# Optimization experiments

Hardware: AMD Instinct MI355X
Metric: run time of the kernel (lower is better)

## Reference

```python
import jax, jax.numpy as jnp
import numpy as np

B, N, H, NH = 1024, 101, 128, 8
HD = H // NH
EPS = 1e-5  # torch LayerNorm default


def _xavier(k, shape):
    fan_in, fan_out = shape
    lim = float(np.sqrt(6.0 / (fan_in + fan_out)))
    return jax.random.uniform(k, shape, jnp.float32, -lim, lim)


def setup_inputs() -> dict:
    key = jax.random.key(0)
    ks = jax.random.split(key, 12)
    return {
        "encoder_inputs": jax.random.normal(ks[0], (B, N, H), jnp.float32),
        "pool": jax.random.normal(ks[1], (B, H), jnp.float32),
        "capacity": jnp.ones((B, 1), jnp.float32),
        "demand": jax.random.uniform(ks[2], (B, N), jnp.float32),
        "fc_w": _xavier(ks[3], (H + 1, H)),      # nn.Linear(hidden+1, hidden, bias=False), stored [in,out]
        "fc1_w": _xavier(ks[4], (H, H)),
        "dec_ln_g": jnp.ones((H,), jnp.float32),
        "dec_ln_b": jnp.zeros((H,), jnp.float32),
        "wq": _xavier(ks[5], (H, H)),             # TransformerAttention q/k/v/out projections
        "wk": _xavier(ks[6], (H, H)),
        "wv": _xavier(ks[7], (H, H)),
        "wo": _xavier(ks[8], (H, H)),
        "kp_w": _xavier(ks[9], (H, H)),           # pointer self.k
        "ptr_ln_g": jnp.ones((H,), jnp.float32),
        "ptr_ln_b": jnp.zeros((H,), jnp.float32),
        "n_steps": 120,
        "T": 1,
        "greedy": 1,
    }


def _ln(x, g, b):
    mu = x.mean(-1, keepdims=True)
    v = ((x - mu) ** 2).mean(-1, keepdims=True)
    return (x - mu) * jax.lax.rsqrt(v + EPS) * g + b


def _forward(encoder_inputs, pool, capacity, demand, fc_w, fc1_w, dec_ln_g, dec_ln_b,
             wq, wk, wv, wo, kp_w, ptr_ln_g, ptr_ln_b, n_steps, T):
    b, n, h = encoder_inputs.shape
    # context projections are loop-invariant -> hoist out of the decode loop
    Kh = (encoder_inputs @ wk).reshape(b, n, NH, HD)
    Vh = (encoder_inputs @ wv).reshape(b, n, NH, HD)
    Kp = encoder_inputs @ kp_w            # [B,N,H] pointer keys
    pool_proc = pool @ fc1_w              # [B,H]
    ar = jnp.arange(n)
    arB = jnp.arange(b)
    inv_sqrt_hd = 1.0 / jnp.sqrt(jnp.float32(HD))
    inv_sqrt_h = 1.0 / jnp.sqrt(jnp.float32(h))

    def step(carry, i):
        mask1, cap, idx, inp = carry
        # decoder input: fc([emb, remaining_cap]) + fc1(pool), LayerNorm
        d = jnp.concatenate([inp, cap], -1) @ fc_w + pool_proc
        d = _ln(d, dec_ln_g, dec_ln_b)
        # ---- update_mask ----
        hit = (ar[None, :] == idx[:, None]) & (idx[:, None] != 0)
        mask1 = jnp.where((i > 0) & hit, 1.0, mask1)
        infeas = (mask1[:, 1:] > 0) | (demand[:, 1:] > cap)      # customers
        any_feas = jnp.any(~infeas, axis=-1)
        depot_m = jnp.where(i == 0, True, (idx == 0) & any_feas)  # mask depot if at depot & feasible cust exists
        all_cust = jnp.all(infeas, axis=-1)
        depot_m = jnp.where(all_cust, False, depot_m)             # only depot allowed if no feasible customer
        mb = jnp.concatenate([depot_m[:, None], infeas], axis=1)  # [B,N] bool, True = masked
        # ---- TransformerAttention (mhalayer) ----
        Qh = (d @ wq).reshape(b, NH, HD)
        logit = jnp.einsum('bhd,bnhd->bhn', Qh, Kh) * inv_sqrt_hd
        logit = jnp.where(mb[:, None, :], -jnp.inf, logit)
        attn = jax.nn.softmax(logit, axis=-1)
        x = jnp.einsum('bhn,bnhd->bhd', attn, Vh).reshape(b, h) @ wo
        # ---- pointer compatibility ----
        xn = _ln(x, ptr_ln_g, ptr_ln_b)
        comp = jnp.einsum('bh,bnh->bn', xn, Kp) * inv_sqrt_h
        comp = jnp.where(mb, -jnp.inf, comp)
        comp = jnp.where(jnp.all(mb, axis=-1, keepdims=True), 0.0, comp)
        p = jax.nn.softmax(comp / T, axis=-1) + 1e-10
        p = p / p.sum(axis=-1, keepdims=True)
        idx = jnp.argmax(p, axis=-1)                              # greedy selection
        lp = jnp.log(jnp.take_along_axis(p, idx[:, None], 1)[:, 0])
        done = mask1[:, 1:].sum(-1) >= (n - 1)
        lp = jnp.where(done, 0.0, lp)
        # ---- update_state (demand lookups via .item() in torch -> stop_gradient) ----
        sel = jax.lax.stop_gradient(jnp.take_along_axis(demand, idx[:, None], 1))
        cap = jnp.where(idx[:, None] == 0, jax.lax.stop_gradient(capacity), cap - sel)
        inp = encoder_inputs[arB, idx]
        return (mask1, cap, idx, inp), (idx, lp)

    init = (jnp.zeros((b, n), jnp.float32), capacity,
            jnp.zeros((b,), jnp.int32), encoder_inputs[:, 0])
    _, (idxs, lps) = jax.lax.scan(step, init, jnp.arange(n_steps))
    last = idxs[-1]
    final = jnp.where(last == 0, -1, 0).astype(jnp.int32)
    actions = jnp.concatenate(
        [jnp.zeros((b, 1), jnp.int32), idxs.T.astype(jnp.int32), final[:, None]], axis=1)
    log_p = lps.sum(0)
    return actions, log_p


def reference(encoder_inputs, pool, capacity, demand, fc_w, fc1_w, dec_ln_g, dec_ln_b,
              wq, wk, wv, wo, kp_w, ptr_ln_g, ptr_ln_b, n_steps, T, greedy):
    # greedy flag: this reference implements the greedy=True path (deterministic argmax).
    return _forward(encoder_inputs, pool, capacity, demand, fc_w, fc1_w, dec_ln_g,
                    dec_ln_b, wq, wk, wv, wo, kp_w, ptr_ln_g, ptr_ln_b,
                    int(n_steps), float(T))
```

## Files before the change

### kernel.cpp

```cpp
#include <hip/hip_runtime.h>
#include <math.h>

constexpr int N_ = 101, H_ = 128;
constexpr int SK = 129;
constexpr float EPS_ = 1e-5f;

constexpr int OFF_KH  = 0;
constexpr int OFF_AT  = 13032;
constexpr int OFF_DRAW = OFF_AT + 816;
constexpr int OFF_DV  = OFF_DRAW + 128;
constexpr int OFF_XV  = OFF_DV + 128;
constexpr int OFF_YR  = OFF_XV + 128;
constexpr int OFF_XN  = OFF_YR + 128;
constexpr int OFF_CP  = OFF_XN + 128;
constexpr int LDS_WORDS = OFF_CP + 128;

#define WSUM(v) { v += __shfl_xor(v,1,64); v += __shfl_xor(v,2,64); v += __shfl_xor(v,4,64); \
                  v += __shfl_xor(v,8,64); v += __shfl_xor(v,16,64); v += __shfl_xor(v,32,64); }
#define WMAX(v) { v = fmaxf(v,__shfl_xor(v,1,64)); v = fmaxf(v,__shfl_xor(v,2,64)); \
                  v = fmaxf(v,__shfl_xor(v,4,64)); v = fmaxf(v,__shfl_xor(v,8,64)); \
                  v = fmaxf(v,__shfl_xor(v,16,64)); v = fmaxf(v,__shfl_xor(v,32,64)); }

__device__ __forceinline__ float rdlane(float v, int l) {
  return __int_as_float(__builtin_amdgcn_readlane(__float_as_int(v), l));
}

__global__ __launch_bounds__(512, 2) void gat_decoder(
    const float* __restrict__ enc, const float* __restrict__ pool,
    const float* __restrict__ capac, const float* __restrict__ dem,
    const float* __restrict__ fcw, const float* __restrict__ fc1w,
    const float* __restrict__ lng, const float* __restrict__ lnb,
    const float* __restrict__ wq, const float* __restrict__ wk,
    const float* __restrict__ wvm, const float* __restrict__ wo,
    const float* __restrict__ kpw, const float* __restrict__ plg,
    const float* __restrict__ plb, const int* __restrict__ tp,
    float* __restrict__ out, int Bv, int ns)
{
  __shared__ float sm[LDS_WORDS];
  const int tid  = threadIdx.x;
  const int b    = blockIdx.x;
  const int lane = tid & 63;
  const int wvid = tid >> 6;
  const int lc   = lane & 15;
  const int sl   = lane >> 4;
  const int col  = wvid * 16 + lc;
  const int n1 = lane, n2 = lane + 64;

  const float NEG_INF = -__builtin_inff();
  int ti = tp[0];
  float Tf = (ti > 1000000 || ti < -1000000) ? __int_as_float((int)ti) : (float)ti;
  const float inv_sqrt_h = 1.0f / sqrtf(128.0f);
  const float PSUM_CONST = 1.0f + (float)N_ * 1e-10f;

  const float* encb = enc + (size_t)b * (N_ * H_);

  float* KH  = sm + OFF_KH;  float* AT = sm + OFF_AT;
  float* DRAW = sm + OFF_DRAW; float* DV = sm + OFF_DV;
  float* XV = sm + OFF_XV;   float* YR = sm + OFF_YR;
  float* XN = sm + OFF_XN;   float* CP = sm + OFF_CP;

  {
    const int j3 = tid & 127;
    const int g3 = __builtin_amdgcn_readfirstlane(tid >> 7);
    const int r03 = g3 * 26, nr3 = (g3 == 3) ? 23 : 26;
    float acc[26];
    #pragma unroll
    for (int t = 0; t < 26; ++t) acc[t] = 0.f;
    for (int k0 = 0; k0 < H_; k0 += 8) {
      float w8[8];
      #pragma unroll
      for (int kk = 0; kk < 8; ++kk) w8[kk] = kpw[(k0 + kk) * H_ + j3];
      #pragma unroll
      for (int t = 0; t < 26; ++t) if (t < nr3) {
        const float* ep = encb + (r03 + t) * H_ + k0;
        #pragma unroll
        for (int kk = 0; kk < 8; ++kk) acc[t] = fmaf(ep[kk], w8[kk], acc[t]);
      }
    }
    #pragma unroll
    for (int t = 0; t < 26; ++t) if (t < nr3) KH[(r03 + t) * SK + j3] = acc[t];
  }
  __syncthreads();
  float kpT[32];
  {
    const int neff = (col < N_) ? col : (N_ - 1);
    const float* src = KH + neff * SK + sl * 32;
    #pragma unroll
    for (int r = 0; r < 32; ++r) kpT[r] = src[r];
  }
  __syncthreads();
  {
    const int j3 = tid & 127;
    const int g3 = __builtin_amdgcn_readfirstlane(tid >> 7);
    const int r03 = g3 * 26, nr3 = (g3 == 3) ? 23 : 26;
    float acc[26];
    #pragma unroll
    for (int t = 0; t < 26; ++t) acc[t] = 0.f;
    for (int k0 = 0; k0 < H_; k0 += 8) {
      float w8[8];
      #pragma unroll
      for (int kk = 0; kk < 8; ++kk) w8[kk] = wk[(k0 + kk) * H_ + j3];
      #pragma unroll
      for (int t = 0; t < 26; ++t) if (t < nr3) {
        const float* ep = encb + (r03 + t) * H_ + k0;
        #pragma unroll
        for (int kk = 0; kk < 8; ++kk) acc[t] = fmaf(ep[kk], w8[kk], acc[t]);
      }
    }
    #pragma unroll
    for (int t = 0; t < 26; ++t) if (t < nr3) KH[(r03 + t) * SK + j3] = acc[t];
  }
  float vh[26];
  {
    const int r0v = sl * 26, nrv = (sl == 3) ? 23 : 26;
    #pragma unroll
    for (int t = 0; t < 26; ++t) vh[t] = 0.f;
    for (int k0 = 0; k0 < H_; k0 += 8) {
      float w8[8];
      #pragma unroll
      for (int kk = 0; kk < 8; ++kk) w8[kk] = wvm[(k0 + kk) * H_ + col];
      #pragma unroll
      for (int t = 0; t < 26; ++t) if (t < nrv) {
        const float* ep = encb + (r0v + t) * H_ + k0;
        #pragma unroll
        for (int kk = 0; kk < 8; ++kk) vh[t] = fmaf(ep[kk], w8[kk], vh[t]);
      }
    }
  }
  float fc_r[32], wq_r[32], wo_r[32];
  #pragma unroll
  for (int r = 0; r < 32; ++r) {
    fc_r[r] = fcw[(sl * 32 + r) * H_ + col];
    wq_r[r] = wq[(sl * 32 + r) * H_ + col];
    wo_r[r] = wo[(sl * 32 + r) * H_ + col];
  }
  const float fcap = fcw[128 * H_ + col];
  float pp;
  {
    const float* pb = pool + (size_t)b * H_;
    float p = 0.f;
    #pragma unroll
    for (int r = 0; r < 32; ++r) p = fmaf(pb[sl * 32 + r], fc1w[(sl * 32 + r) * H_ + col], p);
    p += __shfl_xor(p, 16, 64); p += __shfl_xor(p, 32, 64);
    pp = p;
  }
  const float capv = capac[b];
  float cap = capv, lpsum = 0.f;
  float demA = dem[(size_t)b * N_ + n1];
  float demC = (n2 < N_) ? dem[(size_t)b * N_ + n2] : 0.f;
  const float lngA = lng[n1], lngC = lng[n2 & 127];
  const float lnbA = lnb[n1], lnbC = lnb[n2 & 127];
  const float plgA = plg[n1], plgC = plg[n2 & 127];
  const float plbA = plb[n1], plbC = plb[n2 & 127];
  int vis = 0, pidx = 0;
  bool m1a = false, m1c = false, mbA, mbB;
  {
    bool infA = (n1 >= 1) && (demA > cap);
    bool infB = (n2 >= N_) || (demC > cap);
    bool feasA = (n1 >= 1) && !infA;
    bool feasB = (n2 < N_) && !infB;
    const bool anyf = __any(feasA || feasB);
    mbA = (n1 == 0) ? anyf : infA;
    mbB = infB;
  }
  __syncthreads();

  for (int i = 0; i < ns; ++i) {
    const int pu = __builtin_amdgcn_readfirstlane(pidx);

    {
      const float* ep = encb + (size_t)pu * H_ + sl * 32;
      float p = 0.f;
      #pragma unroll
      for (int r = 0; r < 32; ++r) p = fmaf(fc_r[r], ep[r], p);
      p += __shfl_xor(p, 16, 64); p += __shfl_xor(p, 32, 64);
      p += cap * fcap + pp;
      if (sl == 0) DRAW[col] = p;
    }
    __syncthreads();

    if (wvid == 0) {
      const float DA = DRAW[n1], DC = DRAW[n2 & 127];
      float s1 = DA + DC;
      WSUM(s1);
      const float mu = s1 * (1.f / 128.f);
      const float da = DA - mu, dc = DC - mu;
      float vv = da * da + dc * dc;
      WSUM(vv);
      const float inv = 1.0f / sqrtf(vv * (1.f / 128.f) + EPS_);
      DV[n1] = da * inv * lngA + lnbA;
      DV[n2 & 127] = dc * inv * lngC + lnbC;
    }
    __syncthreads();

    {
      const float4* dv4 = (const float4*)(DV + sl * 32);
      float q = 0.f;
      #pragma unroll
      for (int r4 = 0; r4 < 8; ++r4) {
        const float4 u = dv4[r4];
        q = fmaf(wq_r[r4 * 4 + 0], u.x, q);
        q = fmaf(wq_r[r4 * 4 + 1], u.y, q);
        q = fmaf(wq_r[r4 * 4 + 2], u.z, q);
        q = fmaf(wq_r[r4 * 4 + 3], u.w, q);
      }
      q += __shfl_xor(q, 16, 64); q += __shfl_xor(q, 32, 64);
      const float* k1 = KH + n1 * SK + wvid * 16;
      const float* k2 = KH + ((n2 < N_) ? n2 : n1) * SK + wvid * 16;
      float a1 = 0.f, a2r = 0.f;
      #pragma unroll
      for (int d = 0; d < 16; ++d) {
        const float qdv = rdlane(q, d);
        a1  = fmaf(qdv, k1[d], a1);
        a2r = fmaf(qdv, k2[d], a2r);
      }
      a1 = mbA ? NEG_INF : a1 * 0.25f;
      float a2 = (n2 < N_ && !mbB) ? a2r * 0.25f : NEG_INF;
      float mx = fmaxf(a1, a2);
      WMAX(mx);
      float e1 = expf(a1 - mx);
      float e2 = (n2 < N_) ? expf(a2 - mx) : 0.f;
      float ss = e1 + e2;
      WSUM(ss);
      AT[wvid * N_ + n1] = e1 / ss;
      if (n2 < N_) AT[wvid * N_ + n2] = e2 / ss;
    }
    {
      const float* aw = AT + wvid * N_ + sl * 26;
      const int nrv = (sl == 3) ? 23 : 26;
      float x = 0.f;
      #pragma unroll
      for (int t = 0; t < 26; ++t) if (t < nrv) x = fmaf(aw[t], vh[t], x);
      x += __shfl_xor(x, 16, 64); x += __shfl_xor(x, 32, 64);
      if (sl == 0) XV[col] = x;
    }
    __syncthreads();

    {
      const float4* xp4 = (const float4*)(XV + sl * 32);
      float y = 0.f;
      #pragma unroll
      for (int r4 = 0; r4 < 8; ++r4) {
        const float4 u = xp4[r4];
        y = fmaf(wo_r[r4 * 4 + 0], u.x, y);
        y = fmaf(wo_r[r4 * 4 + 1], u.y, y);
        y = fmaf(wo_r[r4 * 4 + 2], u.z, y);
        y = fmaf(wo_r[r4 * 4 + 3], u.w, y);
      }
      y += __shfl_xor(y, 16, 64); y += __shfl_xor(y, 32, 64);
      if (sl == 0) YR[col] = y;
    }
    __syncthreads();

    if (wvid == 0) {
      const float YA = YR[n1], YC = YR[n2 & 127];
      float s1 = YA + YC;
      WSUM(s1);
      const float mu = s1 * (1.f / 128.f);
      const float da = YA - mu, dc = YC - mu;
      float vv = da * da + dc * dc;
      WSUM(vv);
      const float inv = 1.0f / sqrtf(vv * (1.f / 128.f) + EPS_);
      XN[n1] = da * inv * plgA + plbA;
      XN[n2 & 127] = dc * inv * plgC + plbC;
    }
    __syncthreads();

    {
      const float4* xp4 = (const float4*)(XN + sl * 32);
      float c = 0.f;
      #pragma unroll
      for (int r4 = 0; r4 < 8; ++r4) {
        const float4 u = xp4[r4];
        c = fmaf(kpT[r4 * 4 + 0], u.x, c);
        c = fmaf(kpT[r4 * 4 + 1], u.y, c);
        c = fmaf(kpT[r4 * 4 + 2], u.z, c);
        c = fmaf(kpT[r4 * 4 + 3], u.w, c);
      }
      c += __shfl_xor(c, 16, 64); c += __shfl_xor(c, 32, 64);
      if (sl == 0 && col < N_) CP[col] = c;
    }
    __syncthreads();

    {
      const bool allmb = __all(mbA && mbB);
      float c1 = mbA ? NEG_INF : CP[n1] * inv_sqrt_h / Tf;
      float c2 = (n2 < N_ && !mbB) ? CP[n2 & 127] * inv_sqrt_h / Tf : NEG_INF;
      if (allmb) { c1 = 0.f; c2 = (n2 < N_) ? 0.f : NEG_INF; }
      float bv = c1; int bi = n1;
      if (c2 > bv) { bv = c2; bi = n2; }
      #pragma unroll
      for (int o = 32; o; o >>= 1) {
        float ov = __shfl_xor(bv, o, 64);
        int   oi = __shfl_xor(bi, o, 64);
        if (ov > bv || (ov == bv && oi < bi)) { bv = ov; bi = oi; }
      }
      float e1 = expf(c1 - bv);
      float e2 = (n2 < N_) ? expf(c2 - bv) : 0.f;
      float ss = e1 + e2;
      WSUM(ss);
      float lp = logf((1.0f / ss + 1e-10f) / PSUM_CONST);
      if (vis >= N_ - 1) lp = 0.f;
      lpsum += lp;
      const int bis = __builtin_amdgcn_readfirstlane(bi);
      const float dsel = (bis < 64) ? rdlane(demA, bis) : rdlane(demC, bis - 64);
      cap = (bis == 0) ? capv : (cap - dsel);
      if (bis != 0) {
        const bool newly = ((bis == n1) && !m1a) || ((bis == n2) && !m1c);
        if (__any(newly)) vis += 1;
        m1a = m1a || (bis == n1);
        m1c = m1c || (bis == n2);
      }
      bool infA = (n1 >= 1) && (m1a || demA > cap);
      bool infB = (n2 >= N_) || m1c || (demC > cap);
      bool feasA = (n1 >= 1) && !infA;
      bool feasB = (n2 < N_) && !infB;
      const bool anyf = __any(feasA || feasB);
      const bool depot_m = anyf && (bis == 0);
      mbA = (n1 == 0) ? depot_m : infA;
      mbB = infB;
      pidx = bis;
      if (wvid == 0 && lane == 0) out[(size_t)b * (ns + 2) + 1 + i] = (float)bis;
    }
  }

  if (wvid == 0 && lane == 0) {
    out[(size_t)b * (ns + 2)] = 0.f;
    out[(size_t)b * (ns + 2) + ns + 1] = (pidx == 0) ? -1.f : 0.f;
    out[(size_t)Bv * (ns + 2) + b] = lpsum;
  }
}

extern "C" void kernel_launch(void* const* d_in, const int* in_sizes, int n_in,
                              void* d_out, int out_size, void* d_ws, size_t ws_size,
                              hipStream_t stream) {
  const int Bv = in_sizes[0] / (N_ * H_);
  const int ns = out_size / Bv - 3;
  gat_decoder<<<dim3(Bv), dim3(512), 0, stream>>>(
      (const float*)d_in[0],  (const float*)d_in[1],  (const float*)d_in[2],
      (const float*)d_in[3],  (const float*)d_in[4],  (const float*)d_in[5],
      (const float*)d_in[6],  (const float*)d_in[7],  (const float*)d_in[8],
      (const float*)d_in[9],  (const float*)d_in[10], (const float*)d_in[11],
      (const float*)d_in[12], (const float*)d_in[13], (const float*)d_in[14],
      (const int*)d_in[16],
      (float*)d_out, Bv, ns);
}
```

Before: 2.977 ms.

## Fold LayerNorm affine into downstream weights to drop two barriers per step

Each LayerNorm's gamma/beta is folded into the following projection weights (wq and the pointer keys), and each wave applies the mean/inv-std correction algebraically after the matvec on the raw vector. Every wave now computes the LN statistics redundantly instead of wave 0 writing a normalized vector to LDS, which removes two __syncthreads and two LDS buffers per decode step. The trade is redundant reductions in all waves and a small change in floating-point rounding order, which could flip argmax ties.

```diff
diff --git a/kernel.cpp b/kernel.cpp
--- a/kernel.cpp
+++ b/kernel.cpp
@@ -8,11 +8,9 @@
 constexpr int OFF_KH  = 0;
 constexpr int OFF_AT  = 13032;
 constexpr int OFF_DRAW = OFF_AT + 816;
-constexpr int OFF_DV  = OFF_DRAW + 128;
-constexpr int OFF_XV  = OFF_DV + 128;
+constexpr int OFF_XV  = OFF_DRAW + 128;
 constexpr int OFF_YR  = OFF_XV + 128;
-constexpr int OFF_XN  = OFF_YR + 128;
-constexpr int OFF_CP  = OFF_XN + 128;
+constexpr int OFF_CP  = OFF_YR + 128;
 constexpr int LDS_WORDS = OFF_CP + 128;
 
 #define WSUM(v) { v += __shfl_xor(v,1,64); v += __shfl_xor(v,2,64); v += __shfl_xor(v,4,64); \
@@ -55,9 +53,9 @@
   const float* encb = enc + (size_t)b * (N_ * H_);
 
   float* KH  = sm + OFF_KH;  float* AT = sm + OFF_AT;
-  float* DRAW = sm + OFF_DRAW; float* DV = sm + OFF_DV;
+  float* DRAW = sm + OFF_DRAW;
   float* XV = sm + OFF_XV;   float* YR = sm + OFF_YR;
-  float* XN = sm + OFF_XN;   float* CP = sm + OFF_CP;
+  float* CP = sm + OFF_CP;
 
   {
     const int j3 = tid & 127;
@@ -81,12 +79,23 @@
     for (int t = 0; t < 26; ++t) if (t < nr3) KH[(r03 + t) * SK + j3] = acc[t];
   }
   __syncthreads();
-  float kpT[32];
+  float kpT[32], kps, cpb;
   {
     const int neff = (col < N_) ? col : (N_ - 1);
     const float* src = KH + neff * SK + sl * 32;
-    #pragma unroll
-    for (int r = 0; r < 32; ++r) kpT[r] = src[r];
+    float ks = 0.f, cb = 0.f;
+    #pragma unroll
+    for (int r = 0; r < 32; ++r) {
+      const float kv = src[r];
+      const float pg = plg[sl * 32 + r];
+      const float pb2 = plb[sl * 32 + r];
+      ks = fmaf(kv, pg, ks);
+      cb = fmaf(kv, pb2, cb);
+      kpT[r] = kv * pg;
+    }
+    ks += __shfl_xor(ks, 16, 64); ks += __shfl_xor(ks, 32, 64);
+    cb += __shfl_xor(cb, 16, 64); cb += __shfl_xor(cb, 32, 64);
+    kps = ks; cpb = cb;
   }
   __syncthreads();
   {
@@ -127,12 +136,23 @@
       }
     }
   }
-  float fc_r[32], wq_r[32], wo_r[32];
-  #pragma unroll
-  for (int r = 0; r < 32; ++r) {
-    fc_r[r] = fcw[(sl * 32 + r) * H_ + col];
-    wq_r[r] = wq[(sl * 32 + r) * H_ + col];
-    wo_r[r] = wo[(sl * 32 + r) * H_ + col];
+  float fc_r[32], wo_r[32], wq_r[32], wqs, qb;
+  {
+    float ws = 0.f, bsum = 0.f;
+    #pragma unroll
+    for (int r = 0; r < 32; ++r) {
+      fc_r[r] = fcw[(sl * 32 + r) * H_ + col];
+      wo_r[r] = wo[(sl * 32 + r) * H_ + col];
+      const float w = wq[(sl * 32 + r) * H_ + col];
+      const float lg = lng[sl * 32 + r];
+      const float lb = lnb[sl * 32 + r];
+      wq_r[r] = w * lg;
+      ws = fmaf(w, lg, ws);
+      bsum = fmaf(w, lb, bsum);
+    }
+    ws += __shfl_xor(ws, 16, 64); ws += __shfl_xor(ws, 32, 64);
+    bsum += __shfl_xor(bsum, 16, 64); bsum += __shfl_xor(bsum, 32, 64);
+    wqs = ws; qb = bsum;
   }
   const float fcap = fcw[128 * H_ + col];
   float pp;
@@ -148,10 +168,6 @@
   float cap = capv, lpsum = 0.f;
   float demA = dem[(size_t)b * N_ + n1];
   float demC = (n2 < N_) ? dem[(size_t)b * N_ + n2] : 0.f;
-  const float lngA = lng[n1], lngC = lng[n2 & 127];
-  const float lnbA = lnb[n1], lnbC = lnb[n2 & 127];
-  const float plgA = plg[n1], plgC = plg[n2 & 127];
-  const float plbA = plb[n1], plbC = plb[n2 & 127];
   int vis = 0, pidx = 0;
   bool m1a = false, m1c = false, mbA, mbB;
   {
@@ -179,7 +195,7 @@
     }
     __syncthreads();
 
-    if (wvid == 0) {
+    {
       const float DA = DRAW[n1], DC = DRAW[n2 & 127];
       float s1 = DA + DC;
       WSUM(s1);
@@ -188,23 +204,18 @@
       float vv = da * da + dc * dc;
       WSUM(vv);
       const float inv = 1.0f / sqrtf(vv * (1.f / 128.f) + EPS_);
-      DV[n1] = da * inv * lngA + lnbA;
-      DV[n2 & 127] = dc * inv * lngC + lnbC;
-    }
-    __syncthreads();
-
-    {
-      const float4* dv4 = (const float4*)(DV + sl * 32);
-      float q = 0.f;
+      const float4* dv4 = (const float4*)(DRAW + sl * 32);
+      float p = 0.f;
       #pragma unroll
       for (int r4 = 0; r4 < 8; ++r4) {
         const float4 u = dv4[r4];
-        q = fmaf(wq_r[r4 * 4 + 0], u.x, q);
-        q = fmaf(wq_r[r4 * 4 + 1], u.y, q);
-        q = fmaf(wq_r[r4 * 4 + 2], u.z, q);
-        q = fmaf(wq_r[r4 * 4 + 3], u.w, q);
-      }
-      q += __shfl_xor(q, 16, 64); q += __shfl_xor(q, 32, 64);
+        p = fmaf(wq_r[r4 * 4 + 0], u.x, p);
+        p = fmaf(wq_r[r4 * 4 + 1], u.y, p);
+        p = fmaf(wq_r[r4 * 4 + 2], u.z, p);
+        p = fmaf(wq_r[r4 * 4 + 3], u.w, p);
+      }
+      p += __shfl_xor(p, 16, 64); p += __shfl_xor(p, 32, 64);
+      const float q = inv * (p - mu * wqs) + qb;
       const float* k1 = KH + n1 * SK + wvid * 16;
       const float* k2 = KH + ((n2 < N_) ? n2 : n1) * SK + wvid * 16;
       float a1 = 0.f, a2r = 0.f;
@@ -224,8 +235,6 @@
       WSUM(ss);
       AT[wvid * N_ + n1] = e1 / ss;
       if (n2 < N_) AT[wvid * N_ + n2] = e2 / ss;
-    }
-    {
       const float* aw = AT + wvid * N_ + sl * 26;
       const int nrv = (sl == 3) ? 23 : 26;
       float x = 0.f;
@@ -252,7 +261,7 @@
     }
     __syncthreads();
 
-    if (wvid == 0) {
+    {
       const float YA = YR[n1], YC = YR[n2 & 127];
       float s1 = YA + YC;
       WSUM(s1);
@@ -261,24 +270,19 @@
       float vv = da * da + dc * dc;
       WSUM(vv);
       const float inv = 1.0f / sqrtf(vv * (1.f / 128.f) + EPS_);
-      XN[n1] = da * inv * plgA + plbA;
-      XN[n2 & 127] = dc * inv * plgC + plbC;
-    }
-    __syncthreads();
-
-    {
-      const float4* xp4 = (const float4*)(XN + sl * 32);
+      const float4* yp4 = (const float4*)(YR + sl * 32);
       float c = 0.f;
       #pragma unroll
       for (int r4 = 0; r4 < 8; ++r4) {
-        const float4 u = xp4[r4];
+        const float4 u = yp4[r4];
         c = fmaf(kpT[r4 * 4 + 0], u.x, c);
         c = fmaf(kpT[r4 * 4 + 1], u.y, c);
         c = fmaf(kpT[r4 * 4 + 2], u.z, c);
         c = fmaf(kpT[r4 * 4 + 3], u.w, c);
       }
       c += __shfl_xor(c, 16, 64); c += __shfl_xor(c, 32, 64);
-      if (sl == 0 && col < N_) CP[col] = c;
+      const float comp = inv * (c - mu * kps) + cpb;
+      if (sl == 0 && col < N_) CP[col] = comp;
     }
     __syncthreads();
 
```

Measured after the change: 3.013 ms. Within noise of the previous version (+1.2%).
